# Kernel tuning notes

Hardware: AMD Instinct MI355X
Metric: run time of the kernel (lower is better)

Reference implementation:

```python
import jax, jax.numpy as jnp
import numpy as np

D_MODEL = 1024
NHEAD = 16
D_FF = 4 * D_MODEL
EPS = 1e-5


def layer_norm(x, gamma, beta):
    mu = jnp.mean(x, axis=-1, keepdims=True)
    var = jnp.mean(jnp.square(x - mu), axis=-1, keepdims=True)
    return (x - mu) * jax.lax.rsqrt(var + EPS) * gamma + beta


def setup_inputs() -> dict:
    key = jax.random.key(0)
    ks = jax.random.split(key, 12)
    B, S, D = 4, 2048, D_MODEL
    s = 1.0 / np.sqrt(D)
    return {
        "x": jax.random.normal(ks[0], (B, S, D), jnp.float32),
        "wq": jax.random.normal(ks[1], (D, D), jnp.float32) * s,
        "wk": jax.random.normal(ks[2], (D, D), jnp.float32) * s,
        "wv": jax.random.normal(ks[3], (D, D), jnp.float32) * s,
        "wo": jax.random.normal(ks[4], (D, D), jnp.float32) * s,
        "bo": jnp.zeros((D,), jnp.float32),
        "ln1_g": jnp.ones((D,), jnp.float32),
        "ln1_b": jnp.zeros((D,), jnp.float32),
        "ln2_g": jnp.ones((D,), jnp.float32),
        "ln2_b": jnp.zeros((D,), jnp.float32),
        "w1": jax.random.normal(ks[5], (D, D_FF), jnp.float32) * s,
        "b1": jnp.zeros((D_FF,), jnp.float32),
        "w2": jax.random.normal(ks[6], (D_FF, D), jnp.float32) * (1.0 / np.sqrt(D_FF)),
        "b2": jnp.zeros((D,), jnp.float32),
    }


def reference(x, wq, wk, wv, wo, bo, ln1_g, ln1_b, ln2_g, ln2_b, w1, b1, w2, b2):
    B, S, D = x.shape
    H = NHEAD
    Dh = D // H
    xn = layer_norm(x, ln1_g, ln1_b)
    # projections -> [B, H, S, Dh]
    q = jnp.einsum('bsd,de->bse', xn, wq).reshape(B, S, H, Dh).transpose(0, 2, 1, 3)
    k = jnp.einsum('bsd,de->bse', xn, wk).reshape(B, S, H, Dh).transpose(0, 2, 1, 3)
    v = jnp.einsum('bsd,de->bse', xn, wv).reshape(B, S, H, Dh).transpose(0, 2, 1, 3)
    scores = jnp.einsum('bhsd,bhtd->bhst', q, k) / np.sqrt(Dh)  # [B,H,S,S]
    attn = jax.nn.softmax(scores, axis=-1)
    ctx = jnp.einsum('bhst,bhtd->bhsd', attn, v)
    ctx = ctx.transpose(0, 2, 1, 3).reshape(B, S, D)
    att_out = jnp.einsum('bsd,de->bse', ctx, wo) + bo
    xt = x + att_out
    h = layer_norm(xt, ln2_g, ln2_b)
    ffn = jnp.einsum('bsf,fd->bsd', jax.nn.relu(jnp.einsum('bsd,df->bsf', h, w1) + b1), w2) + b2
    return xt + ffn
```

## Files before the change

### kernel.cpp

```cpp
#include <hip/hip_runtime.h>
#include <stdint.h>

typedef __attribute__((ext_vector_type(8))) __bf16 bf16x8;
typedef __attribute__((ext_vector_type(4))) __bf16 bf16x4;
typedef __attribute__((ext_vector_type(4))) float f32x4;
typedef unsigned short u16;

#define D_MODEL 1024
#define D_FF 4096
#define SEQ 2048
#define NHEAD 16
#define DH 64
#define MROWS 8192

__device__ __forceinline__ u16 f2bf(float f) {
  union { float f; unsigned u; } v; v.f = f;
  unsigned r = v.u + 0x7fffu + ((v.u >> 16) & 1u);
  return (u16)(r >> 16);
}

__device__ __forceinline__ void gload16(const u16* g, u16* l) {
  __builtin_amdgcn_global_load_lds((const __attribute__((address_space(1))) void*)(g),
                                   (__attribute__((address_space(3))) void*)(l),
                                   16, 0, 0);
}

__device__ __forceinline__ void block_bar() {
  asm volatile("" ::: "memory");
  __builtin_amdgcn_s_barrier();
  asm volatile("" ::: "memory");
}

template <int N>
__device__ __forceinline__ void wait_vm() {
  if constexpr (N == 6)      asm volatile("s_waitcnt vmcnt(6)" ::: "memory");
  else if constexpr (N == 4) asm volatile("s_waitcnt vmcnt(4)" ::: "memory");
  else                       asm volatile("s_waitcnt vmcnt(0)" ::: "memory");
}

__global__ __launch_bounds__(256)
void wconv_kernel(const float* __restrict__ W, u16* __restrict__ Wt, int K, int N,
                  float scale) {
  __shared__ u16 t[32][33];
  const int tid = threadIdx.x, tx = tid & 31, ty = tid >> 5;
  const int n0 = blockIdx.x * 32, k0 = blockIdx.y * 32;
#pragma unroll
  for (int i = 0; i < 4; ++i) {
    int k = ty + i * 8;
    t[k][tx] = f2bf(W[(size_t)(k0 + k) * N + n0 + tx] * scale);
  }
  __syncthreads();
#pragma unroll
  for (int i = 0; i < 4; ++i) {
    int n = ty + i * 8;
    Wt[(size_t)(n0 + n) * K + k0 + tx] = t[tx][n];
  }
}

__global__ __launch_bounds__(256)
void ln_kernel(const float* __restrict__ x, u16* __restrict__ out,
               const float* __restrict__ g, const float* __restrict__ beta) {
  const int row = blockIdx.x, tid = threadIdx.x;
  const float4 v = reinterpret_cast<const float4*>(x + (size_t)row * D_MODEL)[tid];
  float s = v.x + v.y + v.z + v.w;
#pragma unroll
  for (int off = 32; off; off >>= 1) s += __shfl_down(s, off);
  __shared__ float red[8];
  if ((tid & 63) == 0) red[tid >> 6] = s;
  __syncthreads();
  const float mu = (red[0] + red[1] + red[2] + red[3]) * (1.0f / D_MODEL);
  const float dx = v.x - mu, dy = v.y - mu, dz = v.z - mu, dw = v.w - mu;
  float sq = dx * dx + dy * dy + dz * dz + dw * dw;
#pragma unroll
  for (int off = 32; off; off >>= 1) sq += __shfl_down(sq, off);
  if ((tid & 63) == 0) red[4 + (tid >> 6)] = sq;
  __syncthreads();
  const float var = (red[4] + red[5] + red[6] + red[7]) * (1.0f / D_MODEL);
  const float rs = rsqrtf(var + 1e-5f);
  const float4 gv = reinterpret_cast<const float4*>(g)[tid];
  const float4 bv = reinterpret_cast<const float4*>(beta)[tid];
  ushort4 ov;
  ov.x = f2bf(dx * rs * gv.x + bv.x);
  ov.y = f2bf(dy * rs * gv.y + bv.y);
  ov.z = f2bf(dz * rs * gv.z + bv.z);
  ov.w = f2bf(dw * rs * gv.w + bv.w);
  reinterpret_cast<ushort4*>(out + (size_t)row * D_MODEL)[tid] = ov;
}

template <int BM, int EPI>
__global__ __launch_bounds__(512, 2)
void gemm8p_kernel(const u16* __restrict__ A, const u16* __restrict__ Bt,
                   int N, int K,
                   const float* __restrict__ bias,
                   const float* __restrict__ res,
                   float* __restrict__ outf, u16* __restrict__ outb,
                   u16* __restrict__ outb2, u16* __restrict__ outb3) {
  constexpr int WM = BM / 2;
  constexpr int MREP = WM / 16;
  constexpr int MI = MREP / 4;
  constexpr int ACH = BM / 64;
  constexpr int VN = (BM == 256) ? 6 : 4;
  __shared__ __align__(16) u16 Al[2][BM * 64];
  __shared__ __align__(16) u16 Bl[2][256 * 64];
  const int tid = threadIdx.x, lane = tid & 63, wave = tid >> 6;
  const int wr = wave >> 2, wc = wave & 3;
  const int l16 = lane & 15, g8 = lane >> 4;
  const int srw = lane >> 3;
  const int scl = ((lane & 7) ^ (lane >> 3)) * 8;
  const int swz = (l16 & 7) << 3;
  const int mBase = blockIdx.y * BM, nBase = blockIdx.x * 256;
  const int nt = K >> 6;

  f32x4 acc[MREP][4];
#pragma unroll
  for (int mi = 0; mi < MREP; ++mi)
#pragma unroll
    for (int nj = 0; nj < 4; ++nj) acc[mi][nj] = f32x4{0.f, 0.f, 0.f, 0.f};

  auto stageChunk = [&](int tile, int c) {
    if (tile >= nt) return;
    const int buf = tile & 1;
    if (c < ACH) {
      const int r0 = c * 64 + wave * 8;
      gload16(A + (size_t)(mBase + r0 + srw) * K + tile * 64 + scl,
              &Al[buf][r0 * 64]);
    } else {
      const int r0 = (c - ACH) * 64 + wave * 8;
      gload16(Bt + (size_t)(nBase + r0 + srw) * K + tile * 64 + scl,
              &Bl[buf][r0 * 64]);
    }
  };

  constexpr int STO256[16] = {1,1, 2,2, 2,2, 2,2, 2,2, 3,3, 3,3, 3,3};
  constexpr int STC256[16] = {1,3, 4,5, 6,7, 0,2, 1,3, 4,5, 6,7, 0,2};
  constexpr int STO128[16] = {1,1, 2,2, 2,2, 0,0, 2,2, 3,3, 3,3, 0,0};
  constexpr int STC128[16] = {0,1, 2,3, 4,5, -1,-1, 0,1, 2,3, 4,5, -1,-1};

  constexpr int P0_256[8] = {4,5,6,7,0,2,1,3};
  constexpr int P1_256[6] = {4,5,6,7,0,2};
  constexpr int P0_128[6] = {2,3,4,5,0,1};
  constexpr int P1_128[4] = {2,3,4,5};
  if constexpr (BM == 256) {
#pragma unroll
    for (int i = 0; i < 8; ++i) stageChunk(0, P0_256[i]);
#pragma unroll
    for (int i = 0; i < 6; ++i) stageChunk(1, P1_256[i]);
  } else {
#pragma unroll
    for (int i = 0; i < 6; ++i) stageChunk(0, P0_128[i]);
#pragma unroll
    for (int i = 0; i < 4; ++i) stageChunk(1, P1_128[i]);
  }
  wait_vm<VN>();
  block_bar();

  for (int T = 0; T < nt; T += 2) {
    bf16x8 bfr[4][2];
#pragma unroll
    for (int p = 0; p < 8; ++p) {
      const int q = p & 3;
      const int buf = p >> 2;
      if (q == 0) {
#pragma unroll
        for (int nj = 0; nj < 4; ++nj)
#pragma unroll
          for (int ks = 0; ks < 2; ++ks) {
            const int rb = wc * 64 + nj * 16 + l16;
            bfr[nj][ks] = *reinterpret_cast<const bf16x8*>(
                &Bl[buf][rb * 64 + ((ks * 32 + g8 * 8) ^ swz)]);
          }
      }
      bf16x8 af[MI][2];
#pragma unroll
      for (int i = 0; i < MI; ++i)
#pragma unroll
        for (int ks = 0; ks < 2; ++ks) {
          const int ra = wr * WM + (q * MI + i) * 16 + l16;
          af[i][ks] = *reinterpret_cast<const bf16x8*>(
              &Al[buf][ra * 64 + ((ks * 32 + g8 * 8) ^ swz)]);
        }
      if constexpr (BM == 256) {
        stageChunk(T + STO256[2 * p], STC256[2 * p]);
        stageChunk(T + STO256[2 * p + 1], STC256[2 * p + 1]);
      } else {
        if (STC128[2 * p] >= 0) {
          stageChunk(T + STO128[2 * p], STC128[2 * p]);
          stageChunk(T + STO128[2 * p + 1], STC128[2 * p + 1]);
        }
      }
      block_bar();
      __builtin_amdgcn_s_setprio(1);
#pragma unroll
      for (int i = 0; i < MI; ++i)
#pragma unroll
        for (int nj = 0; nj < 4; ++nj)
#pragma unroll
          for (int ks = 0; ks < 2; ++ks)
            acc[q * MI + i][nj] = __builtin_amdgcn_mfma_f32_16x16x32_bf16(
                af[i][ks], bfr[nj][ks], acc[q * MI + i][nj], 0, 0, 0);
      __builtin_amdgcn_s_setprio(0);
      if (p == 3) {
        if (T + 2 < nt) wait_vm<VN>(); else wait_vm<0>();
      } else if (p == 7) {
        wait_vm<VN>();
      }
      block_bar();
    }
  }

#pragma unroll
  for (int mi = 0; mi < MREP; ++mi)
#pragma unroll
    for (int nj = 0; nj < 4; ++nj) {
      const int colB = wc * 64 + nj * 16 + l16;
      const int row0 = mBase + wr * WM + mi * 16 + g8 * 4;
      if (EPI == 4) {
        const int seg = nBase >> 10;
        const int c = (nBase & 1023) + colB;
        if (seg == 2) {
          const int bi = row0 >> 11, s = row0 & 2047;
          ushort4 pk;
          pk.x = f2bf(acc[mi][nj][0]);
          pk.y = f2bf(acc[mi][nj][1]);
          pk.z = f2bf(acc[mi][nj][2]);
          pk.w = f2bf(acc[mi][nj][3]);
          *reinterpret_cast<ushort4*>(outb3 + ((size_t)(bi << 10) + c) * SEQ + s) = pk;
        } else {
          u16* o = (seg == 0) ? outb : outb2;
#pragma unroll
          for (int r = 0; r < 4; ++r)
            o[(size_t)(row0 + r) * D_MODEL + c] = f2bf(acc[mi][nj][r]);
        }
      } else {
        const int col = nBase + colB;
        const float bv = bias[col];
#pragma unroll
        for (int r = 0; r < 4; ++r) {
          const size_t idx = (size_t)(row0 + r) * N + col;
          const float vv = acc[mi][nj][r];
          if (EPI == 1) {
            outf[idx] = vv + bv + res[idx];
          } else {
            const float tv = vv + bv;
            outb[idx] = f2bf(tv > 0.f ? tv : 0.f);
          }
        }
      }
    }
}

__global__ __launch_bounds__(256)
void attn_kernel(const u16* __restrict__ qb, const u16* __restrict__ kb,
                 const u16* __restrict__ vb, u16* __restrict__ ctx) {
  __shared__ __align__(16) u16 Kl[2][64 * 64];
  __shared__ __align__(16) u16 Vl[2][64 * 64];
  __shared__ __align__(16) u16 Pl[4][32 * 64];
  const int tid = threadIdx.x;
  const int lane = tid & 63, wave = tid >> 6, g8 = lane >> 4, l16 = lane & 15;
  const int b = blockIdx.y >> 4, h = blockIdx.y & 15;
  const int q0 = blockIdx.x * 128 + wave * 32;
  const size_t rowB = (size_t)b * SEQ;
  const int colH = h * DH;
  const size_t vtBase = (size_t)(b * 1024 + colH) * SEQ;
  const int srw = lane >> 3;
  const int scl = ((lane & 7) ^ (lane >> 3)) * 8;
  const int cswz = (l16 & 7) * 8;

  bf16x8 qf[2][2];
#pragma unroll
  for (int m = 0; m < 2; ++m)
#pragma unroll
    for (int ks = 0; ks < 2; ++ks)
      qf[m][ks] = *reinterpret_cast<const bf16x8*>(
          qb + (rowB + q0 + m * 16 + l16) * D_MODEL + colH + ks * 32 + g8 * 8);

  float mi[2] = {-1e30f, -1e30f}, li[2] = {0.f, 0.f};
  f32x4 o[2][4];
#pragma unroll
  for (int m = 0; m < 2; ++m)
#pragma unroll
    for (int nt = 0; nt < 4; ++nt) o[m][nt] = f32x4{0.f, 0.f, 0.f, 0.f};

  auto stageKV = [&](int t0, int buf) {
    if (t0 >= SEQ) return;
#pragma unroll
    for (int i = 0; i < 2; ++i) {
      const int r0 = wave * 16 + i * 8;
      gload16(kb + (rowB + t0 + r0 + srw) * D_MODEL + colH + scl, &Kl[buf][r0 * 64]);
      gload16(vb + vtBase + (size_t)(r0 + srw) * SEQ + t0 + scl, &Vl[buf][r0 * 64]);
    }
  };

  stageKV(0, 0);
  wait_vm<0>();
  block_bar();

  int buf = 0;
  for (int t0 = 0; t0 < SEQ; t0 += 64, buf ^= 1) {
    stageKV(t0 + 64, buf ^ 1);

    f32x4 st[2][4];
#pragma unroll
    for (int m = 0; m < 2; ++m)
#pragma unroll
      for (int kt = 0; kt < 4; ++kt) st[m][kt] = f32x4{0.f, 0.f, 0.f, 0.f};
#pragma unroll
    for (int kt = 0; kt < 4; ++kt) {
      const bf16x8 kf0 = *reinterpret_cast<const bf16x8*>(
          &Kl[buf][(kt * 16 + l16) * 64 + ((g8 * 8) ^ cswz)]);
      const bf16x8 kf1 = *reinterpret_cast<const bf16x8*>(
          &Kl[buf][(kt * 16 + l16) * 64 + ((32 + g8 * 8) ^ cswz)]);
#pragma unroll
      for (int m = 0; m < 2; ++m) {
        st[m][kt] = __builtin_amdgcn_mfma_f32_16x16x32_bf16(kf0, qf[m][0], st[m][kt], 0, 0, 0);
        st[m][kt] = __builtin_amdgcn_mfma_f32_16x16x32_bf16(kf1, qf[m][1], st[m][kt], 0, 0, 0);
      }
    }

    float alpha[2];
#pragma unroll
    for (int m = 0; m < 2; ++m) {
      float pmax = st[m][0][0];
#pragma unroll
      for (int kt = 0; kt < 4; ++kt)
#pragma unroll
        for (int r = 0; r < 4; ++r) pmax = fmaxf(pmax, st[m][kt][r]);
      pmax = fmaxf(pmax, __shfl_xor(pmax, 16));
      pmax = fmaxf(pmax, __shfl_xor(pmax, 32));
      const float mnew = fmaxf(mi[m], pmax);
      alpha[m] = __builtin_amdgcn_exp2f(mi[m] - mnew);
      mi[m] = mnew;
      float sum = 0.f;
#pragma unroll
      for (int kt = 0; kt < 4; ++kt) {
        bf16x4 pk;
#pragma unroll
        for (int r = 0; r < 4; ++r) {
          const float p = __builtin_amdgcn_exp2f(st[m][kt][r] - mnew);
          sum += p;
          pk[r] = (__bf16)p;
        }
        const int row = m * 16 + l16;
        *reinterpret_cast<bf16x4*>(
            &Pl[wave][row * 64 + ((kt * 16 + g8 * 4) ^ cswz)]) = pk;
      }
      sum += __shfl_xor(sum, 16);
      sum += __shfl_xor(sum, 32);
      li[m] = li[m] * alpha[m] + sum;
    }

#pragma unroll
    for (int m = 0; m < 2; ++m) {
      f32x4 al;
#pragma unroll
      for (int r = 0; r < 4; ++r) al[r] = __shfl(alpha[m], g8 * 4 + r);
#pragma unroll
      for (int nt = 0; nt < 4; ++nt) {
        f32x4 t = o[m][nt];
        t[0] *= al[0]; t[1] *= al[1]; t[2] *= al[2]; t[3] *= al[3];
        o[m][nt] = t;
      }
    }

    bf16x8 pf[2][2];
#pragma unroll
    for (int m = 0; m < 2; ++m)
#pragma unroll
      for (int ks = 0; ks < 2; ++ks)
        pf[m][ks] = *reinterpret_cast<const bf16x8*>(
            &Pl[wave][(m * 16 + l16) * 64 + ((ks * 32 + g8 * 8) ^ cswz)]);
#pragma unroll
    for (int nt = 0; nt < 4; ++nt) {
      const bf16x8 vf0 = *reinterpret_cast<const bf16x8*>(
          &Vl[buf][(nt * 16 + l16) * 64 + ((g8 * 8) ^ cswz)]);
      const bf16x8 vf1 = *reinterpret_cast<const bf16x8*>(
          &Vl[buf][(nt * 16 + l16) * 64 + ((32 + g8 * 8) ^ cswz)]);
#pragma unroll
      for (int m = 0; m < 2; ++m) {
        o[m][nt] = __builtin_amdgcn_mfma_f32_16x16x32_bf16(pf[m][0], vf0, o[m][nt], 0, 0, 0);
        o[m][nt] = __builtin_amdgcn_mfma_f32_16x16x32_bf16(pf[m][1], vf1, o[m][nt], 0, 0, 0);
      }
    }

    wait_vm<0>();
    block_bar();
  }

#pragma unroll
  for (int m = 0; m < 2; ++m) {
    f32x4 ld;
#pragma unroll
    for (int r = 0; r < 4; ++r) ld[r] = 1.0f / __shfl(li[m], g8 * 4 + r);
#pragma unroll
    for (int nt = 0; nt < 4; ++nt)
#pragma unroll
      for (int r = 0; r < 4; ++r) {
        const __bf16 v = (__bf16)(o[m][nt][r] * ld[r]);
        ctx[(rowB + q0 + m * 16 + g8 * 4 + r) * D_MODEL + colH + nt * 16 + l16] =
            __builtin_bit_cast(u16, v);
      }
  }
}

extern "C" void kernel_launch(void* const* d_in, const int* in_sizes, int n_in,
                              void* d_out, int out_size, void* d_ws, size_t ws_size,
                              hipStream_t stream) {
  const float* x   = (const float*)d_in[0];
  const float* wq  = (const float*)d_in[1];
  const float* wk  = (const float*)d_in[2];
  const float* wv  = (const float*)d_in[3];
  const float* wo  = (const float*)d_in[4];
  const float* bo  = (const float*)d_in[5];
  const float* l1g = (const float*)d_in[6];
  const float* l1b = (const float*)d_in[7];
  const float* l2g = (const float*)d_in[8];
  const float* l2b = (const float*)d_in[9];
  const float* w1  = (const float*)d_in[10];
  const float* b1  = (const float*)d_in[11];
  const float* w2  = (const float*)d_in[12];
  const float* b2  = (const float*)d_in[13];
  float* outp = (float*)d_out;

  uint8_t* ws = (uint8_t*)d_ws;
  const size_t MB = 1024 * 1024;
  u16* wqkvt = (u16*)(ws + 0 * MB);
  u16* wqt   = wqkvt;
  u16* wkt   = (u16*)(ws + 2 * MB);
  u16* wvt   = (u16*)(ws + 4 * MB);
  u16* wot   = (u16*)(ws + 6 * MB);
  u16* w1t   = (u16*)(ws + 8 * MB);
  u16* w2t   = (u16*)(ws + 16 * MB);
  u16* xn    = (u16*)(ws + 24 * MB);
  u16* qbuf  = (u16*)(ws + 40 * MB);
  u16* kbuf  = (u16*)(ws + 56 * MB);
  u16* vbufT = (u16*)(ws + 72 * MB);
  u16* ctx   = xn;
  u16* hbuf  = qbuf;
  u16* ffh   = kbuf;

  dim3 blk(256);
  dim3 blk5(512);

  wconv_kernel<<<dim3(32, 32), blk, 0, stream>>>(wq, wqt, 1024, 1024, 0.18033688011112042f);
  wconv_kernel<<<dim3(32, 32), blk, 0, stream>>>(wk, wkt, 1024, 1024, 1.0f);
  wconv_kernel<<<dim3(32, 32), blk, 0, stream>>>(wv, wvt, 1024, 1024, 1.0f);
  wconv_kernel<<<dim3(32, 32), blk, 0, stream>>>(wo, wot, 1024, 1024, 1.0f);
  wconv_kernel<<<dim3(128, 32), blk, 0, stream>>>(w1, w1t, 1024, 4096, 1.0f);
  wconv_kernel<<<dim3(32, 128), blk, 0, stream>>>(w2, w2t, 4096, 1024, 1.0f);

  ln_kernel<<<MROWS, blk, 0, stream>>>(x, xn, l1g, l1b);

  gemm8p_kernel<128, 4><<<dim3(12, 64), blk5, 0, stream>>>(
      xn, wqkvt, 3072, 1024, nullptr, nullptr, nullptr, qbuf, kbuf, vbufT);

  attn_kernel<<<dim3(16, 64), blk, 0, stream>>>(qbuf, kbuf, vbufT, ctx);

  gemm8p_kernel<128, 1><<<dim3(4, 64), blk5, 0, stream>>>(
      ctx, wot, 1024, 1024, bo, x, outp, nullptr, nullptr, nullptr);

  ln_kernel<<<MROWS, blk, 0, stream>>>(outp, hbuf, l2g, l2b);

  gemm8p_kernel<256, 2><<<dim3(16, 32), blk5, 0, stream>>>(
      hbuf, w1t, 4096, 1024, b1, nullptr, nullptr, ffh, nullptr, nullptr);

  gemm8p_kernel<128, 1><<<dim3(4, 64), blk5, 0, stream>>>(
      ffh, w2t, 1024, 4096, b2, outp, outp, nullptr, nullptr, nullptr);
}
```

Baseline: 553.2 us.

## Rework BM=128 GEMM pipeline into 4 phases and add lazy softmax rescale

For the BM=128 GEMM variant, the k-loop now runs four phases per two k-tiles instead of eight, each computing two M-fragments. It issues three staged loads per phase with a new prefetch schedule and a vmcnt(3) wait, aiming to cut barriers and improve load/compute overlap. In the attention kernel, the running max and the output rescale are updated only when some lane's new block max exceeds the old max by more than 8 (log2 units), skipping exp and multiply work otherwise. The lazy rescale keeps probabilities up to 2^8 before normalization, which relies on fp32 range and slightly changes bf16 rounding of P.

```diff
diff --git a/kernel.cpp b/kernel.cpp
--- a/kernel.cpp
+++ b/kernel.cpp
@@ -35,6 +35,7 @@
 __device__ __forceinline__ void wait_vm() {
   if constexpr (N == 6)      asm volatile("s_waitcnt vmcnt(6)" ::: "memory");
   else if constexpr (N == 4) asm volatile("s_waitcnt vmcnt(4)" ::: "memory");
+  else if constexpr (N == 3) asm volatile("s_waitcnt vmcnt(3)" ::: "memory");
   else                       asm volatile("s_waitcnt vmcnt(0)" ::: "memory");
 }
 
@@ -97,9 +98,9 @@
                    u16* __restrict__ outb2, u16* __restrict__ outb3) {
   constexpr int WM = BM / 2;
   constexpr int MREP = WM / 16;
-  constexpr int MI = MREP / 4;
+  constexpr int MI = 2;
   constexpr int ACH = BM / 64;
-  constexpr int VN = (BM == 256) ? 6 : 4;
+  constexpr int VN = (BM == 256) ? 6 : 3;
   __shared__ __align__(16) u16 Al[2][BM * 64];
   __shared__ __align__(16) u16 Bl[2][256 * 64];
   const int tid = threadIdx.x, lane = tid & 63, wave = tid >> 6;
@@ -131,80 +132,122 @@
     }
   };
 
-  constexpr int STO256[16] = {1,1, 2,2, 2,2, 2,2, 2,2, 3,3, 3,3, 3,3};
-  constexpr int STC256[16] = {1,3, 4,5, 6,7, 0,2, 1,3, 4,5, 6,7, 0,2};
-  constexpr int STO128[16] = {1,1, 2,2, 2,2, 0,0, 2,2, 3,3, 3,3, 0,0};
-  constexpr int STC128[16] = {0,1, 2,3, 4,5, -1,-1, 0,1, 2,3, 4,5, -1,-1};
-
-  constexpr int P0_256[8] = {4,5,6,7,0,2,1,3};
-  constexpr int P1_256[6] = {4,5,6,7,0,2};
-  constexpr int P0_128[6] = {2,3,4,5,0,1};
-  constexpr int P1_128[4] = {2,3,4,5};
   if constexpr (BM == 256) {
-#pragma unroll
-    for (int i = 0; i < 8; ++i) stageChunk(0, P0_256[i]);
-#pragma unroll
-    for (int i = 0; i < 6; ++i) stageChunk(1, P1_256[i]);
+    constexpr int P0[8] = {4,5,6,7,0,2,1,3};
+    constexpr int P1[6] = {4,5,6,7,0,2};
+#pragma unroll
+    for (int i = 0; i < 8; ++i) stageChunk(0, P0[i]);
+#pragma unroll
+    for (int i = 0; i < 6; ++i) stageChunk(1, P1[i]);
   } else {
-#pragma unroll
-    for (int i = 0; i < 6; ++i) stageChunk(0, P0_128[i]);
-#pragma unroll
-    for (int i = 0; i < 4; ++i) stageChunk(1, P1_128[i]);
+    constexpr int P0[6] = {2,3,4,5,0,1};
+    constexpr int P1[3] = {2,3,4};
+#pragma unroll
+    for (int i = 0; i < 6; ++i) stageChunk(0, P0[i]);
+#pragma unroll
+    for (int i = 0; i < 3; ++i) stageChunk(1, P1[i]);
   }
   wait_vm<VN>();
   block_bar();
 
-  for (int T = 0; T < nt; T += 2) {
-    bf16x8 bfr[4][2];
-#pragma unroll
-    for (int p = 0; p < 8; ++p) {
-      const int q = p & 3;
-      const int buf = p >> 2;
-      if (q == 0) {
-#pragma unroll
-        for (int nj = 0; nj < 4; ++nj)
+  if constexpr (BM == 256) {
+    constexpr int STO[16] = {1,1, 2,2, 2,2, 2,2, 2,2, 3,3, 3,3, 3,3};
+    constexpr int STC[16] = {1,3, 4,5, 6,7, 0,2, 1,3, 4,5, 6,7, 0,2};
+    for (int T = 0; T < nt; T += 2) {
+      bf16x8 bfr[4][2];
+#pragma unroll
+      for (int p = 0; p < 8; ++p) {
+        const int q = p & 3;
+        const int buf = p >> 2;
+        if (q == 0) {
+#pragma unroll
+          for (int nj = 0; nj < 4; ++nj)
+#pragma unroll
+            for (int ks = 0; ks < 2; ++ks) {
+              const int rb = wc * 64 + nj * 16 + l16;
+              bfr[nj][ks] = *reinterpret_cast<const bf16x8*>(
+                  &Bl[buf][rb * 64 + ((ks * 32 + g8 * 8) ^ swz)]);
+            }
+        }
+        bf16x8 af[MI][2];
+#pragma unroll
+        for (int i = 0; i < MI; ++i)
 #pragma unroll
           for (int ks = 0; ks < 2; ++ks) {
-            const int rb = wc * 64 + nj * 16 + l16;
-            bfr[nj][ks] = *reinterpret_cast<const bf16x8*>(
-                &Bl[buf][rb * 64 + ((ks * 32 + g8 * 8) ^ swz)]);
+            const int ra = wr * WM + (q * MI + i) * 16 + l16;
+            af[i][ks] = *reinterpret_cast<const bf16x8*>(
+                &Al[buf][ra * 64 + ((ks * 32 + g8 * 8) ^ swz)]);
           }
-      }
-      bf16x8 af[MI][2];
-#pragma unroll
-      for (int i = 0; i < MI; ++i)
-#pragma unroll
-        for (int ks = 0; ks < 2; ++ks) {
-          const int ra = wr * WM + (q * MI + i) * 16 + l16;
-          af[i][ks] = *reinterpret_cast<const bf16x8*>(
-              &Al[buf][ra * 64 + ((ks * 32 + g8 * 8) ^ swz)]);
-        }
-      if constexpr (BM == 256) {
-        stageChunk(T + STO256[2 * p], STC256[2 * p]);
-        stageChunk(T + STO256[2 * p + 1], STC256[2 * p + 1]);
-      } else {
-        if (STC128[2 * p] >= 0) {
-          stageChunk(T + STO128[2 * p], STC128[2 * p]);
-          stageChunk(T + STO128[2 * p + 1], STC128[2 * p + 1]);
-        }
-      }
-      block_bar();
-      __builtin_amdgcn_s_setprio(1);
-#pragma unroll
-      for (int i = 0; i < MI; ++i)
-#pragma unroll
-        for (int nj = 0; nj < 4; ++nj)
-#pragma unroll
-          for (int ks = 0; ks < 2; ++ks)
-            acc[q * MI + i][nj] = __builtin_amdgcn_mfma_f32_16x16x32_bf16(
-                af[i][ks], bfr[nj][ks], acc[q * MI + i][nj], 0, 0, 0);
-      __builtin_amdgcn_s_setprio(0);
-      if (p == 3) {
-        if (T + 2 < nt) wait_vm<VN>(); else wait_vm<0>();
-      } else if (p == 7) {
-        wait_vm<VN>();
-      }
-      block_bar();
+        stageChunk(T + STO[2 * p], STC[2 * p]);
+        stageChunk(T + STO[2 * p + 1], STC[2 * p + 1]);
+        block_bar();
+        __builtin_amdgcn_s_setprio(1);
+#pragma unroll
+        for (int i = 0; i < MI; ++i)
+#pragma unroll
+          for (int nj = 0; nj < 4; ++nj)
+#pragma unroll
+            for (int ks = 0; ks < 2; ++ks)
+              acc[q * MI + i][nj] = __builtin_amdgcn_mfma_f32_16x16x32_bf16(
+                  af[i][ks], bfr[nj][ks], acc[q * MI + i][nj], 0, 0, 0);
+        __builtin_amdgcn_s_setprio(0);
+        if (p == 3) {
+          if (T + 2 < nt) wait_vm<VN>(); else wait_vm<0>();
+        } else if (p == 7) {
+          wait_vm<VN>();
+        }
+        block_bar();
+      }
+    }
+  } else {
+    constexpr int STO[12] = {1,1,1, 2,2,2, 2,2,2, 3,3,3};
+    constexpr int STC[12] = {5,0,1, 2,3,4, 5,0,1, 2,3,4};
+    for (int T = 0; T < nt; T += 2) {
+      bf16x8 bfr[4][2];
+#pragma unroll
+      for (int p = 0; p < 4; ++p) {
+        const int q = p & 1;
+        const int buf = p >> 1;
+        if (q == 0) {
+#pragma unroll
+          for (int nj = 0; nj < 4; ++nj)
+#pragma unroll
+            for (int ks = 0; ks < 2; ++ks) {
+              const int rb = wc * 64 + nj * 16 + l16;
+              bfr[nj][ks] = *reinterpret_cast<const bf16x8*>(
+                  &Bl[buf][rb * 64 + ((ks * 32 + g8 * 8) ^ swz)]);
+            }
+        }
+        bf16x8 af[MI][2];
+#pragma unroll
+        for (int i = 0; i < MI; ++i)
+#pragma unroll
+          for (int ks = 0; ks < 2; ++ks) {
+            const int ra = wr * WM + (q * MI + i) * 16 + l16;
+            af[i][ks] = *reinterpret_cast<const bf16x8*>(
+                &Al[buf][ra * 64 + ((ks * 32 + g8 * 8) ^ swz)]);
+          }
+        stageChunk(T + STO[3 * p], STC[3 * p]);
+        stageChunk(T + STO[3 * p + 1], STC[3 * p + 1]);
+        stageChunk(T + STO[3 * p + 2], STC[3 * p + 2]);
+        block_bar();
+        __builtin_amdgcn_s_setprio(1);
+#pragma unroll
+        for (int i = 0; i < MI; ++i)
+#pragma unroll
+          for (int nj = 0; nj < 4; ++nj)
+#pragma unroll
+            for (int ks = 0; ks < 2; ++ks)
+              acc[q * MI + i][nj] = __builtin_amdgcn_mfma_f32_16x16x32_bf16(
+                  af[i][ks], bfr[nj][ks], acc[q * MI + i][nj], 0, 0, 0);
+        __builtin_amdgcn_s_setprio(0);
+        if (p == 1) {
+          if (T + 2 < nt) wait_vm<VN>(); else wait_vm<0>();
+        } else if (p == 3) {
+          if (T + 3 < nt) wait_vm<VN>(); else wait_vm<0>();
+        }
+        block_bar();
+      }
     }
   }
 
@@ -318,6 +361,7 @@
     }
 
     float alpha[2];
+    bool dor[2];
 #pragma unroll
     for (int m = 0; m < 2; ++m) {
       float pmax = st[m][0][0];
@@ -327,16 +371,20 @@
         for (int r = 0; r < 4; ++r) pmax = fmaxf(pmax, st[m][kt][r]);
       pmax = fmaxf(pmax, __shfl_xor(pmax, 16));
       pmax = fmaxf(pmax, __shfl_xor(pmax, 32));
-      const float mnew = fmaxf(mi[m], pmax);
-      alpha[m] = __builtin_amdgcn_exp2f(mi[m] - mnew);
-      mi[m] = mnew;
+      dor[m] = !__all(pmax - mi[m] <= 8.0f);
+      alpha[m] = 1.0f;
+      if (dor[m]) {
+        const float mnew = fmaxf(mi[m], pmax);
+        alpha[m] = __builtin_amdgcn_exp2f(mi[m] - mnew);
+        mi[m] = mnew;
+      }
       float sum = 0.f;
 #pragma unroll
       for (int kt = 0; kt < 4; ++kt) {
         bf16x4 pk;
 #pragma unroll
         for (int r = 0; r < 4; ++r) {
-          const float p = __builtin_amdgcn_exp2f(st[m][kt][r] - mnew);
+          const float p = __builtin_amdgcn_exp2f(st[m][kt][r] - mi[m]);
           sum += p;
           pk[r] = (__bf16)p;
         }
@@ -351,14 +399,16 @@
 
 #pragma unroll
     for (int m = 0; m < 2; ++m) {
-      f32x4 al;
-#pragma unroll
-      for (int r = 0; r < 4; ++r) al[r] = __shfl(alpha[m], g8 * 4 + r);
-#pragma unroll
-      for (int nt = 0; nt < 4; ++nt) {
-        f32x4 t = o[m][nt];
-        t[0] *= al[0]; t[1] *= al[1]; t[2] *= al[2]; t[3] *= al[3];
-        o[m][nt] = t;
+      if (dor[m]) {
+        f32x4 al;
+#pragma unroll
+        for (int r = 0; r < 4; ++r) al[r] = __shfl(alpha[m], g8 * 4 + r);
+#pragma unroll
+        for (int nt = 0; nt < 4; ++nt) {
+          f32x4 t = o[m][nt];
+          t[0] *= al[0]; t[1] *= al[1]; t[2] *= al[2]; t[3] *= al[3];
+          o[m][nt] = t;
+        }
       }
     }
 
```

Measured after the change: 548.2 us. About the same (-0.9%).
